# Performance work log

Measured on AMD Instinct MI355X. Metric: run time of the kernel, lower is better.

The kernel has to match this reference:

```python
import jax, jax.numpy as jnp
import numpy as np

# Grid config from init_kwargs
VX, VY = 0.1, 0.1
XMIN, YMIN, ZMIN, XMAX, YMAX, ZMAX = 0.0, -25.6, -3.0, 51.2, 25.6, 3.0
H = int(round((XMAX - XMIN) / VX))  # 512
W = int(round((YMAX - YMIN) / VY))  # 512
SIGMA = 1.5   # gaussian std in voxel units
R = 3         # splat window radius -> 7x7 kernel


def _pose0to1(pose0, pose1):
    # ego-motion: pose1^{-1} @ pose0, per batch element
    return jnp.linalg.inv(pose1) @ pose0


def _transform(xyz, pose):
    # xyz: [B,N,3], pose: [B,4,4] -> xyz @ R^T + t
    Rm = pose[:, :3, :3]
    t = pose[:, :3, 3]
    return jnp.einsum('bnd,bed->bne', xyz, Rm) + t[:, None, :]


def _voxelize(xyz):
    # continuous voxel coords + integer pillar indices + in-range mask
    px = (xyz[..., 0] - XMIN) / VX
    py = (xyz[..., 1] - YMIN) / VY
    ix = jnp.floor(px).astype(jnp.int32)
    iy = jnp.floor(py).astype(jnp.int32)
    valid = (ix >= 0) & (ix < H) & (iy >= 0) & (iy < W) & \
            (xyz[..., 2] >= ZMIN) & (xyz[..., 2] < ZMAX)
    return px, py, ix, iy, valid


def _gauss_heatmap(px, py, ix, iy, valid):
    # Splat a gaussian (max-composited) around every valid radar pillar.
    B, M = px.shape
    offs = jnp.arange(-R, R + 1)
    dx, dy = jnp.meshgrid(offs, offs, indexing='ij')      # [K,K]
    gx = ix[:, :, None, None] + dx                        # [B,M,K,K]
    gy = iy[:, :, None, None] + dy
    cellx = gx.astype(px.dtype) + 0.5
    celly = gy.astype(py.dtype) + 0.5
    d2 = (cellx - px[:, :, None, None]) ** 2 + (celly - py[:, :, None, None]) ** 2
    val = jnp.exp(-d2 / (2.0 * SIGMA * SIGMA))
    inb = (gx >= 0) & (gx < H) & (gy >= 0) & (gy < W) & valid[:, :, None, None]
    bidx = jnp.arange(B, dtype=jnp.int32)[:, None, None, None]
    flat = jnp.where(inb, bidx * (H * W) + gx * W + gy, B * H * W)  # dummy seg for invalid
    heat = jax.ops.segment_max(val.reshape(-1), flat.reshape(-1),
                               num_segments=B * H * W + 1)
    heat = jnp.maximum(heat[:B * H * W], 0.0).reshape(B, H, W)
    return heat


def _gather(heat, ix, iy, valid):
    # per-point gaussian score = heatmap at the point's pillar
    B = heat.shape[0]
    hf = heat.reshape(B, -1)
    idx = jnp.clip(ix, 0, H - 1) * W + jnp.clip(iy, 0, W - 1)
    s = jnp.take_along_axis(hf, idx, axis=1)
    return jnp.where(valid, s, 0.0)


def _forward(pc0, pc1, radar_pc0, radar_pc1, pose0, pose1):
    # pose computed under no_grad in the original -> stop_gradient
    pose_0to1 = jax.lax.stop_gradient(_pose0to1(pose0, pose1))
    tpc0 = _transform(pc0, pose_0to1)
    trad0_xyz = _transform(radar_pc0[..., :3], pose_0to1)
    # dynamic pillar voxelization (BEV coords)
    _, _, l0x, l0y, l0v = _voxelize(tpc0)
    _, _, l1x, l1y, l1v = _voxelize(pc1)
    r0px, r0py, r0x, r0y, r0v = _voxelize(trad0_xyz)
    r1px, r1py, r1x, r1y, r1v = _voxelize(radar_pc1[..., :3])
    # gaussian maps from radar pillars, scored for lidar + radar points
    heat0 = _gauss_heatmap(r0px, r0py, r0x, r0y, r0v)
    heat1 = _gauss_heatmap(r1px, r1py, r1x, r1y, r1v)
    lidar0 = _gather(heat0, l0x, l0y, l0v)   # [B,N]
    radar0 = _gather(heat0, r0x, r0y, r0v)   # [B,M]
    lidar1 = _gather(heat1, l1x, l1y, l1v)
    radar1 = _gather(heat1, r1x, r1y, r1v)
    return jnp.concatenate([lidar0, radar0, lidar1, radar1], axis=1)


def setup_inputs() -> dict:
    key = jax.random.key(0)
    ks = jax.random.split(key, 8)
    B, N, M = 8, 262144, 8192
    lo = jnp.array([XMIN, YMIN, ZMIN], dtype=jnp.float32)
    hi = jnp.array([XMAX, YMAX, ZMAX], dtype=jnp.float32)
    pc0 = jax.random.uniform(ks[0], (B, N, 3), dtype=jnp.float32) * (hi - lo) + lo
    pc1 = jax.random.uniform(ks[1], (B, N, 3), dtype=jnp.float32) * (hi - lo) + lo
    rxyz0 = jax.random.uniform(ks[2], (B, M, 3), dtype=jnp.float32) * (hi - lo) + lo
    rxyz1 = jax.random.uniform(ks[3], (B, M, 3), dtype=jnp.float32) * (hi - lo) + lo
    radar_pc0 = jnp.concatenate([rxyz0, jax.random.normal(ks[4], (B, M, 3), dtype=jnp.float32)], axis=-1)
    radar_pc1 = jnp.concatenate([rxyz1, jax.random.normal(ks[5], (B, M, 3), dtype=jnp.float32)], axis=-1)

    def mk_pose(k):
        t = jax.random.uniform(k, (B, 3), minval=-0.5, maxval=0.5, dtype=jnp.float32)
        eye = jnp.tile(jnp.eye(4, dtype=jnp.float32)[None], (B, 1, 1))
        return eye.at[:, :3, 3].set(t)

    pose0 = mk_pose(ks[6])
    pose1 = mk_pose(ks[7])
    return {"pc0": pc0, "pc1": pc1, "radar_pc0": radar_pc0,
            "radar_pc1": radar_pc1, "pose0": pose0, "pose1": pose1}


def reference(pc0, pc1, radar_pc0, radar_pc1, pose0, pose1):
    return _forward(pc0, pc1, radar_pc0, radar_pc1, pose0, pose1)
```

## Files before the change

### kernel.cpp

```cpp
#include <hip/hip_runtime.h>
#include <math.h>

#define GH 512
#define GW 512
#define GHW (GH * GW)
#define RR 3
#define SH 16
#define SSHIFT 4
#define NSTRIP (GH / SH)
#define SCAP 1024


__device__ __forceinline__ void compute_pose(const float* __restrict__ P0,
                                             const float* __restrict__ P1,
                                             float* __restrict__ T) {
    double a00 = P1[0], a01 = P1[1], a02 = P1[2],  t1x = P1[3];
    double a10 = P1[4], a11 = P1[5], a12 = P1[6],  t1y = P1[7];
    double a20 = P1[8], a21 = P1[9], a22 = P1[10], t1z = P1[11];
    double c00 = a11 * a22 - a12 * a21;
    double c01 = a12 * a20 - a10 * a22;
    double c02 = a10 * a21 - a11 * a20;
    double det = a00 * c00 + a01 * c01 + a02 * c02;
    double id = 1.0 / det;
    double r00 = c00 * id;
    double r01 = (a02 * a21 - a01 * a22) * id;
    double r02 = (a01 * a12 - a02 * a11) * id;
    double r10 = c01 * id;
    double r11 = (a00 * a22 - a02 * a20) * id;
    double r12 = (a02 * a10 - a00 * a12) * id;
    double r20 = c02 * id;
    double r21 = (a01 * a20 - a00 * a21) * id;
    double r22 = (a00 * a11 - a01 * a10) * id;

    double b00 = P0[0], b01 = P0[1], b02 = P0[2],  t0x = P0[3];
    double b10 = P0[4], b11 = P0[5], b12 = P0[6],  t0y = P0[7];
    double b20 = P0[8], b21 = P0[9], b22 = P0[10], t0z = P0[11];
    double dx = t0x - t1x, dy = t0y - t1y, dz = t0z - t1z;

    T[0]  = (float)(r00 * b00 + r01 * b10 + r02 * b20);
    T[1]  = (float)(r00 * b01 + r01 * b11 + r02 * b21);
    T[2]  = (float)(r00 * b02 + r01 * b12 + r02 * b22);
    T[3]  = (float)(r00 * dx + r01 * dy + r02 * dz);
    T[4]  = (float)(r10 * b00 + r11 * b10 + r12 * b20);
    T[5]  = (float)(r10 * b01 + r11 * b11 + r12 * b21);
    T[6]  = (float)(r10 * b02 + r11 * b12 + r12 * b22);
    T[7]  = (float)(r10 * dx + r11 * dy + r12 * dz);
    T[8]  = (float)(r20 * b00 + r21 * b10 + r22 * b20);
    T[9]  = (float)(r20 * b01 + r21 * b11 + r22 * b21);
    T[10] = (float)(r20 * b02 + r21 * b12 + r22 * b22);
    T[11] = (float)(r20 * dx + r21 * dy + r22 * dz);
}

__device__ __forceinline__ void voxelize_xyz(float x, float y, float z,
                                             const float* __restrict__ T,
                                             float& px, float& py,
                                             int& ix, int& iy, bool& valid) {
    if (T) {
        float nx = T[0] * x + T[1] * y + T[2] * z + T[3];
        float ny = T[4] * x + T[5] * y + T[6] * z + T[7];
        float nz = T[8] * x + T[9] * y + T[10] * z + T[11];
        x = nx; y = ny; z = nz;
    }
    px = (x - 0.0f) * 10.0f;
    py = (y - (-25.6f)) * 10.0f;
    ix = (int)floorf(px);
    iy = (int)floorf(py);
    valid = (ix >= 0) & (ix < GH) & (iy >= 0) & (iy < GW) &
            (z >= -3.0f) & (z < 3.0f);
}

__global__ __launch_bounds__(256)
void heat_strip_kernel(const float* __restrict__ radar0,
                       const float* __restrict__ radar1,
                       const float* __restrict__ pose0,
                       const float* __restrict__ pose1,
                       float* __restrict__ heat0,
                       float* __restrict__ heat1,
                       int B, int M) {
    __shared__ int strip[SH * GW];
    __shared__ float2 sp[SCAP];
    __shared__ float Tsh[12];
    __shared__ int sn;

    const int tid = threadIdx.x;
    const int blk = blockIdx.x;
    const int b = blk % B;
    const int map = (blk / B) & 1;
    const int sx = blk / (2 * B);
    const int x0 = sx << SSHIFT;

    if (tid == 0) {
        sn = 0;
        if (map == 0) compute_pose(pose0 + b * 16, pose1 + b * 16, Tsh);
    }
    {
        const int4 z4 = make_int4(0, 0, 0, 0);
        for (int c4 = tid * 4; c4 < SH * GW; c4 += 1024)
            *reinterpret_cast<int4*>(&strip[c4]) = z4;
    }
    __syncthreads();

    const float* radar = map ? radar1 : radar0;
    const float* T = map ? nullptr : Tsh;
    const float2* pv = reinterpret_cast<const float2*>(radar + (size_t)b * M * 6);

    for (int i = tid; i < M; i += 256) {
        float2 fxy = pv[3 * i];
        float2 fzw = pv[3 * i + 1];
        float px, py; int ix, iy; bool valid;
        voxelize_xyz(fxy.x, fxy.y, fzw.x, T, px, py, ix, iy, valid);
        if (!valid) continue;
        if (ix < x0 - RR || ix > x0 + SH - 1 + RR) continue;
        int slot = atomicAdd(&sn, 1);
        if (slot < SCAP) sp[slot] = make_float2(px, py);
    }
    __syncthreads();

    int n = sn; if (n > SCAP) n = SCAP;
    const int total = n * 49;
    for (int t = tid; t < total; t += 256) {
        int pi = t / 49;
        int c = t - pi * 49;
        float px = sp[pi].x;
        float py = sp[pi].y;
        int ix = (int)floorf(px);
        int iy = (int)floorf(py);
        int dx = c / 7 - RR;
        int dy = c - (c / 7) * 7 - RR;
        int gx = ix + dx, gy = iy + dy;
        if (gx < x0 || gx >= x0 + SH || gy < 0 || gy >= GW) continue;
        float ddx = ((float)gx + 0.5f) - px;
        float ddy = ((float)gy + 0.5f) - py;
        float d2 = ddx * ddx + ddy * ddy;
        float val = expf(-d2 / 4.5f);
        atomicMax(&strip[(gx - x0) * GW + gy], __float_as_int(val));
    }
    __syncthreads();

    float* heat = map ? heat1 : heat0;
    float* hb = heat + (size_t)b * GHW + (size_t)x0 * GW;
    for (int c4 = tid * 4; c4 < SH * GW; c4 += 1024) {
        int4 iv = *reinterpret_cast<const int4*>(&strip[c4]);
        float4 fv;
        fv.x = __int_as_float(iv.x);
        fv.y = __int_as_float(iv.y);
        fv.z = __int_as_float(iv.z);
        fv.w = __int_as_float(iv.w);
        *reinterpret_cast<float4*>(hb + c4) = fv;
    }
}

__global__ __launch_bounds__(256)
void gather_fused_kernel(const float* __restrict__ pc0,
                         const float* __restrict__ pc1,
                         const float* __restrict__ radar0,
                         const float* __restrict__ radar1,
                         const float* __restrict__ pose0,
                         const float* __restrict__ pose1,
                         const float* __restrict__ heat0,
                         const float* __restrict__ heat1,
                         float* __restrict__ out,
                         int N, int M) {
    __shared__ float Tsh[12];
    const int row_len = 2 * N + 2 * M;
    const int b = blockIdx.x;
    const int base = blockIdx.y * 2048 + threadIdx.x;

    if (threadIdx.x == 0) compute_pose(pose0 + b * 16, pose1 + b * 16, Tsh);
    __syncthreads();

    const float* hb0 = heat0 + (size_t)b * GHW;
    const float* hb1 = heat1 + (size_t)b * GHW;
    const float* Tb = Tsh;

    float xs[8], ys[8], zs[8];
    const float* Ts[8];
    const float* hbs[8];
    bool live[8];

    #pragma unroll
    for (int k = 0; k < 8; k++) {
        int r = base + k * 256;
        live[k] = (r < row_len);
        if (!live[k]) continue;
        const float* p;
        const float* T = nullptr;
        const float* hb;
        if (r < N) {
            p = pc0 + ((size_t)b * N + r) * 3;
            T = Tb;
            hb = hb0;
        } else if (r < N + M) {
            p = radar0 + ((size_t)b * M + (r - N)) * 6;
            T = Tb;
            hb = hb0;
        } else if (r < 2 * N + M) {
            p = pc1 + ((size_t)b * N + (r - N - M)) * 3;
            hb = hb1;
        } else {
            p = radar1 + ((size_t)b * M + (r - 2 * N - M)) * 6;
            hb = hb1;
        }
        xs[k] = __builtin_nontemporal_load(p + 0);
        ys[k] = __builtin_nontemporal_load(p + 1);
        zs[k] = __builtin_nontemporal_load(p + 2);
        Ts[k] = T;
        hbs[k] = hb;
    }

    float v[8];
    #pragma unroll
    for (int k = 0; k < 8; k++) {
        if (!live[k]) continue;
        float px, py; int ix, iy; bool valid;
        voxelize_xyz(xs[k], ys[k], zs[k], Ts[k], px, py, ix, iy, valid);
        v[k] = 0.0f;
        if (valid) v[k] = hbs[k][ix * GW + iy];
    }

    #pragma unroll
    for (int k = 0; k < 8; k++) {
        if (!live[k]) continue;
        int r = base + k * 256;
        __builtin_nontemporal_store(v[k], out + (size_t)b * row_len + r);
    }
}

extern "C" void kernel_launch(void* const* d_in, const int* in_sizes, int n_in,
                              void* d_out, int out_size, void* d_ws, size_t ws_size,
                              hipStream_t stream) {
    const float* pc0      = (const float*)d_in[0];
    const float* pc1      = (const float*)d_in[1];
    const float* radar0   = (const float*)d_in[2];
    const float* radar1   = (const float*)d_in[3];
    const float* pose0    = (const float*)d_in[4];
    const float* pose1    = (const float*)d_in[5];
    float* out = (float*)d_out;

    int B = in_sizes[4] / 16;
    int N = in_sizes[0] / (B * 3);
    int M = in_sizes[2] / (B * 6);
    int row_len = 2 * N + 2 * M;

    float* heat0 = (float*)d_ws;
    float* heat1 = heat0 + (size_t)B * GHW;

    int nblk = 2 * B * NSTRIP;
    heat_strip_kernel<<<nblk, 256, 0, stream>>>(
        radar0, radar1, pose0, pose1, heat0, heat1, B, M);

    dim3 ggrid(B, (row_len + 2047) / 2048);
    gather_fused_kernel<<<ggrid, 256, 0, stream>>>(
        pc0, pc1, radar0, radar1, pose0, pose1, heat0, heat1, out, N, M);
}
```

Measured before the change: 161.4 us.

## Voxelize radar points once grid-wide in a cooperative kernel before strip splatting

Replaces the per-strip redundant voxelization, where every strip block transformed all M radar points, with a cooperative kernel. All blocks first voxelize every point once into a workspace buffer, then synchronize across the grid, and each strip block scans the compact precomputed (px,py) array with float4 loads. This removes repeated pose transforms and 24-byte point reads per strip, at the cost of a grid-wide barrier and cooperative launch constraints. It also caps pose storage at 8 batches and assumes M is even.

```diff
diff --git a/kernel.cpp b/kernel.cpp
--- a/kernel.cpp
+++ b/kernel.cpp
@@ -1,5 +1,8 @@
 #include <hip/hip_runtime.h>
+#include <hip/hip_cooperative_groups.h>
 #include <math.h>
+
+namespace cg = cooperative_groups;
 
 #define GH 512
 #define GW 512
@@ -69,50 +72,73 @@
             (z >= -3.0f) & (z < 3.0f);
 }
 
-__global__ __launch_bounds__(256)
-void heat_strip_kernel(const float* __restrict__ radar0,
-                       const float* __restrict__ radar1,
-                       const float* __restrict__ pose0,
-                       const float* __restrict__ pose1,
-                       float* __restrict__ heat0,
-                       float* __restrict__ heat1,
-                       int B, int M) {
+__global__ __launch_bounds__(256, 2)
+void heat_coop_kernel(const float* __restrict__ radar0,
+                      const float* __restrict__ radar1,
+                      const float* __restrict__ pose0,
+                      const float* __restrict__ pose1,
+                      float2* __restrict__ ppxy,
+                      float* __restrict__ heat0,
+                      float* __restrict__ heat1,
+                      int B, int M) {
+    cg::grid_group grid = cg::this_grid();
+
     __shared__ int strip[SH * GW];
     __shared__ float2 sp[SCAP];
-    __shared__ float Tsh[12];
+    __shared__ float Tsh[8][12];
     __shared__ int sn;
 
     const int tid = threadIdx.x;
     const int blk = blockIdx.x;
+    const int nblk = gridDim.x;
+    const int BM = B * M;
+
+    if (tid < B) compute_pose(pose0 + tid * 16, pose1 + tid * 16, &Tsh[tid][0]);
+    if (tid == 0) sn = 0;
+    {
+        const int4 z4 = make_int4(0, 0, 0, 0);
+        for (int c4 = tid * 4; c4 < SH * GW; c4 += 1024)
+            *reinterpret_cast<int4*>(&strip[c4]) = z4;
+    }
+    __syncthreads();
+
+    for (int t = blk * 256 + tid; t < 2 * BM; t += nblk * 256) {
+        int map = t / BM;
+        int rem = t - map * BM;
+        int b = rem / M;
+        const float* radar = map ? radar1 : radar0;
+        const float2* pv = reinterpret_cast<const float2*>(radar + (size_t)rem * 6);
+        float2 fxy = pv[0];
+        float2 fzw = pv[1];
+        float px, py; int ix, iy; bool valid;
+        voxelize_xyz(fxy.x, fxy.y, fzw.x, map ? nullptr : &Tsh[b][0],
+                     px, py, ix, iy, valid);
+        ppxy[t] = valid ? make_float2(px, py) : make_float2(-1e9f, -1e9f);
+    }
+    grid.sync();
+
     const int b = blk % B;
     const int map = (blk / B) & 1;
     const int sx = blk / (2 * B);
     const int x0 = sx << SSHIFT;
 
-    if (tid == 0) {
-        sn = 0;
-        if (map == 0) compute_pose(pose0 + b * 16, pose1 + b * 16, Tsh);
-    }
-    {
-        const int4 z4 = make_int4(0, 0, 0, 0);
-        for (int c4 = tid * 4; c4 < SH * GW; c4 += 1024)
-            *reinterpret_cast<int4*>(&strip[c4]) = z4;
-    }
-    __syncthreads();
-
-    const float* radar = map ? radar1 : radar0;
-    const float* T = map ? nullptr : Tsh;
-    const float2* pv = reinterpret_cast<const float2*>(radar + (size_t)b * M * 6);
-
-    for (int i = tid; i < M; i += 256) {
-        float2 fxy = pv[3 * i];
-        float2 fzw = pv[3 * i + 1];
-        float px, py; int ix, iy; bool valid;
-        voxelize_xyz(fxy.x, fxy.y, fzw.x, T, px, py, ix, iy, valid);
-        if (!valid) continue;
-        if (ix < x0 - RR || ix > x0 + SH - 1 + RR) continue;
-        int slot = atomicAdd(&sn, 1);
-        if (slot < SCAP) sp[slot] = make_float2(px, py);
+    const float4* slice4 =
+        reinterpret_cast<const float4*>(ppxy + (size_t)(map * B + b) * M);
+    const float xlo = (float)(x0 - RR);
+    const float xhi = (float)(x0 + SH - 1 + RR + 1);
+
+    for (int i = tid; i < M / 2; i += 256) {
+        float4 q = slice4[i];
+        int ix0 = (int)floorf(q.x);
+        if (ix0 >= x0 - RR && ix0 <= x0 + SH - 1 + RR) {
+            int slot = atomicAdd(&sn, 1);
+            if (slot < SCAP) sp[slot] = make_float2(q.x, q.y);
+        }
+        int ix1 = (int)floorf(q.z);
+        if (ix1 >= x0 - RR && ix1 <= x0 + SH - 1 + RR) {
+            int slot = atomicAdd(&sn, 1);
+            if (slot < SCAP) sp[slot] = make_float2(q.z, q.w);
+        }
     }
     __syncthreads();
 
@@ -148,6 +174,7 @@
         fv.w = __int_as_float(iv.w);
         *reinterpret_cast<float4*>(hb + c4) = fv;
     }
+    (void)xlo; (void)xhi;
 }
 
 __global__ __launch_bounds__(256)
@@ -244,10 +271,15 @@
 
     float* heat0 = (float*)d_ws;
     float* heat1 = heat0 + (size_t)B * GHW;
+    float2* ppxy = (float2*)(heat1 + (size_t)B * GHW);
 
     int nblk = 2 * B * NSTRIP;
-    heat_strip_kernel<<<nblk, 256, 0, stream>>>(
-        radar0, radar1, pose0, pose1, heat0, heat1, B, M);
+    void* args[] = {
+        (void*)&radar0, (void*)&radar1, (void*)&pose0, (void*)&pose1,
+        (void*)&ppxy, (void*)&heat0, (void*)&heat1, (void*)&B, (void*)&M
+    };
+    hipLaunchCooperativeKernel((const void*)heat_coop_kernel,
+                               dim3(nblk), dim3(256), args, 0, stream);
 
     dim3 ggrid(B, (row_len + 2047) / 2048);
     gather_fused_kernel<<<ggrid, 256, 0, stream>>>(
```

Result: slower. 212.8 us (+31.9%).

## Use wider strips with 1024-thread blocks and early x-reject in heat splat

Applied to the files above, without the earlier changes.

Doubles the strip height to 32 rows and raises the heat kernel's block size to 1024 threads, so there are half as many blocks and each one rescans the radar points half as often. Every thread whose index is below B now computes its batch's pose into a per-batch shared table. The point loop reads x, y and z as scalar floats and rejects points on the x-range test before doing the rest of the transform and validity checks. The risks are the fixed-size pose table of 8 entries, which breaks if B exceeds 8, a larger shared strip (64KB) that limits occupancy, and possible SCAP overflow with more points per strip.

```diff
diff --git a/kernel.cpp b/kernel.cpp
--- a/kernel.cpp
+++ b/kernel.cpp
@@ -5,10 +5,11 @@
 #define GW 512
 #define GHW (GH * GW)
 #define RR 3
-#define SH 16
-#define SSHIFT 4
+#define SH 32
+#define SSHIFT 5
 #define NSTRIP (GH / SH)
 #define SCAP 1024
+#define THR 1024
 
 
 __device__ __forceinline__ void compute_pose(const float* __restrict__ P0,
@@ -69,7 +70,7 @@
             (z >= -3.0f) & (z < 3.0f);
 }
 
-__global__ __launch_bounds__(256)
+__global__ __launch_bounds__(THR)
 void heat_strip_kernel(const float* __restrict__ radar0,
                        const float* __restrict__ radar1,
                        const float* __restrict__ pose0,
@@ -79,7 +80,7 @@
                        int B, int M) {
     __shared__ int strip[SH * GW];
     __shared__ float2 sp[SCAP];
-    __shared__ float Tsh[12];
+    __shared__ float Tsh[8][12];
     __shared__ int sn;
 
     const int tid = threadIdx.x;
@@ -89,28 +90,34 @@
     const int sx = blk / (2 * B);
     const int x0 = sx << SSHIFT;
 
-    if (tid == 0) {
-        sn = 0;
-        if (map == 0) compute_pose(pose0 + b * 16, pose1 + b * 16, Tsh);
-    }
+    if (tid < B) compute_pose(pose0 + tid * 16, pose1 + tid * 16, &Tsh[tid][0]);
+    if (tid == 0) sn = 0;
     {
         const int4 z4 = make_int4(0, 0, 0, 0);
-        for (int c4 = tid * 4; c4 < SH * GW; c4 += 1024)
+        for (int c4 = tid * 4; c4 < SH * GW; c4 += 4 * THR)
             *reinterpret_cast<int4*>(&strip[c4]) = z4;
     }
     __syncthreads();
 
     const float* radar = map ? radar1 : radar0;
-    const float* T = map ? nullptr : Tsh;
-    const float2* pv = reinterpret_cast<const float2*>(radar + (size_t)b * M * 6);
-
-    for (int i = tid; i < M; i += 256) {
-        float2 fxy = pv[3 * i];
-        float2 fzw = pv[3 * i + 1];
-        float px, py; int ix, iy; bool valid;
-        voxelize_xyz(fxy.x, fxy.y, fzw.x, T, px, py, ix, iy, valid);
+    const float* pb = radar + (size_t)b * M * 6;
+    const bool hasT = (map == 0);
+    const float* T = &Tsh[b][0];
+
+    for (int i = tid; i < M; i += THR) {
+        const float* p = pb + (size_t)i * 6;
+        float x = p[0], y = p[1], z = p[2];
+        float nx = hasT ? (T[0] * x + T[1] * y + T[2] * z + T[3]) : x;
+        float px = (nx - 0.0f) * 10.0f;
+        int ix = (int)floorf(px);
+        if (ix < x0 - RR || ix > x0 + SH - 1 + RR) continue;
+        float ny = hasT ? (T[4] * x + T[5] * y + T[6] * z + T[7]) : y;
+        float nz = hasT ? (T[8] * x + T[9] * y + T[10] * z + T[11]) : z;
+        float py = (ny - (-25.6f)) * 10.0f;
+        int iy = (int)floorf(py);
+        bool valid = (ix >= 0) & (ix < GH) & (iy >= 0) & (iy < GW) &
+                     (nz >= -3.0f) & (nz < 3.0f);
         if (!valid) continue;
-        if (ix < x0 - RR || ix > x0 + SH - 1 + RR) continue;
         int slot = atomicAdd(&sn, 1);
         if (slot < SCAP) sp[slot] = make_float2(px, py);
     }
@@ -118,7 +125,7 @@
 
     int n = sn; if (n > SCAP) n = SCAP;
     const int total = n * 49;
-    for (int t = tid; t < total; t += 256) {
+    for (int t = tid; t < total; t += THR) {
         int pi = t / 49;
         int c = t - pi * 49;
         float px = sp[pi].x;
@@ -139,7 +146,7 @@
 
     float* heat = map ? heat1 : heat0;
     float* hb = heat + (size_t)b * GHW + (size_t)x0 * GW;
-    for (int c4 = tid * 4; c4 < SH * GW; c4 += 1024) {
+    for (int c4 = tid * 4; c4 < SH * GW; c4 += 4 * THR) {
         int4 iv = *reinterpret_cast<const int4*>(&strip[c4]);
         float4 fv;
         fv.x = __int_as_float(iv.x);
@@ -246,7 +253,7 @@
     float* heat1 = heat0 + (size_t)B * GHW;
 
     int nblk = 2 * B * NSTRIP;
-    heat_strip_kernel<<<nblk, 256, 0, stream>>>(
+    heat_strip_kernel<<<nblk, THR, 0, stream>>>(
         radar0, radar1, pose0, pose1, heat0, heat1, B, M);
 
     dim3 ggrid(B, (row_len + 2047) / 2048);
```

Result: faster. 144.8 us (-10.3%).
